# Performance work log

Hardware: AMD Instinct MI355X
Metric: run time of the kernel (lower is better)

Reference implementation:

```python
import jax, jax.numpy as jnp
import numpy as np

# Default widths from CWT.__init__: round((exp(linspace(0,2.5,5))-1)*30)+1
WIDTHS = [1, 27, 76, 167, 336]


def _morlet_int_psi():
    """pywt 'morl' wavelet: psi(t)=exp(-t^2/2)*cos(5t) on [-8,8], precision=10,
    integrated (cumulative) as in pywt.integrate_wavelet."""
    precision = 10
    n = 2 ** precision
    lb, ub = -8.0, 8.0
    t = np.linspace(lb, ub, n)
    psi = np.exp(-t ** 2 / 2.0) * np.cos(5.0 * t)
    step = t[1] - t[0]
    int_psi = np.cumsum(psi) * step
    return int_psi, step, lb, ub, n


def _filters(widths):
    """Per-scale resampled integrated wavelet, as in pywt.cwt.
    pywt uses np.convolve(data, int_psi[j][::-1]) (which flips its kernel);
    lax conv is a correlation (no flip), so the equivalent lax kernel is int_psi[j]."""
    int_psi, step, lb, ub, n = _morlet_int_psi()
    filts = []
    for scale in widths:
        j = (np.arange(scale * (ub - lb) + 1) / (scale * step)).astype(np.int64)
        j = j[j < n]
        filts.append(int_psi[j].astype(np.float32))
    return filts

_FILTERS = _filters(WIDTHS)


def _cwt_forward(x):
    # x: [N, T, C]; conv along T, channels independent
    N, T, C = x.shape
    xt = x.transpose(0, 2, 1).reshape(N * C, 1, T)  # [N*C, 1, T]
    outs = []
    for scale, f in zip(WIDTHS, _FILTERS):
        L = f.shape[0]
        k = jnp.asarray(f)[None, None, :]  # [out=1, in=1, L]
        # 'full' convolution: pad L-1 on each side
        conv = jax.lax.conv_general_dilated(xt, k, window_strides=(1,), padding=[(L - 1, L - 1)])  # [N*C,1,T+L-1]
        coef = (-np.sqrt(float(scale))) * jnp.diff(conv, axis=-1)  # [N*C,1,T+L-2]
        d = (coef.shape[-1] - T) / 2.0  # trim to central T samples (pywt)
        lo = int(np.floor(d))
        hi = coef.shape[-1] - int(np.ceil(d))
        coef = coef[..., lo:hi]  # [N*C, 1, T]
        outs.append(coef.reshape(N, C, T))
    out = jnp.stack(outs, axis=0)  # [F, N, C, T]
    return out.transpose(1, 3, 2, 0)  # [N, T, C, F]


def setup_inputs() -> dict:
    key = jax.random.key(0)
    x = jax.random.normal(key, (16, 2048, 64), dtype=jnp.float32)
    return {"x": x}


def reference(x):
    return _cwt_forward(x)
```

## Files before the change

kernel.cpp:

```cpp
#include <hip/hip_runtime.h>
#include <hip/hip_fp16.h>
#include <math.h>

#define NB    16
#define T     2048
#define NC    64
#define NROWS (NB*NC)
#define PADL2 2696
#define XSH_N 7440

#define WTOT_U4 19840

#define WS_XT    (1u<<19)
#define WS_OUTT  ((1u<<19) + (1u<<22))

typedef _Float16 half8  __attribute__((ext_vector_type(8)));
typedef _Float16 half4v __attribute__((ext_vector_type(4)));
typedef float    f32x4  __attribute__((ext_vector_type(4)));

__global__ __launch_bounds__(1024) void cwt_prep(const float* __restrict__ x,
                                                 __half* __restrict__ xT,
                                                 __half* __restrict__ W) {
    __shared__ double ps[1024];
    __shared__ double sc[1024];
    __shared__ float  k32[1024];
    __shared__ float  tile4[4][64 * 65];
    const int tid = threadIdx.x;

    if (blockIdx.x == 0) {
        uint4* W4 = (uint4*)W;
        const uint4 z = make_uint4(0u, 0u, 0u, 0u);
        for (int i = tid; i < WTOT_U4; i += 1024) W4[i] = z;

        const double delta = 16.0 / 1023.0;
        double t = (tid == 1023) ? 8.0 : (-8.0 + delta * (double)tid);
        ps[tid] = exp(-0.5 * t * t) * cos(5.0 * t);
        __syncthreads();

        double* a = ps; double* b = sc;
        for (int off = 1; off < 1024; off <<= 1) {
            double v = a[tid];
            if (tid >= off) v += a[tid - off];
            b[tid] = v;
            __syncthreads();
            double* tmp = a; a = b; b = tmp;
        }
        const double step = ((-8.0 + delta) + 8.0);
        k32[tid] = (float)(a[tid] * step);
        __syncthreads();

        constexpr int SCe[5]   = {336, 167, 76, 27, 1};
        constexpr int KS2[5]   = {5408, 2720, 1248, 480, 64};
        constexpr int WOFFe[5] = {0, 86528, 130048, 150016, 157696};
        constexpr int CLOe[5]  = {0, 42, 65, 77, 83};
        for (int sl = 0; sl < 5; ++sl) {
            const int s = SCe[sl];
            const int L = 16 * s + 1;
            const double c = (double)s * step;
            const float sq = (float)sqrt((double)s);
            const int posoff = PADL2 - 8 * s - 1;
            const int kb0 = posoff - 32 * CLOe[sl];
            __half* wb = W + WOFFe[sl];
            const int Ks = KS2[sl];
            for (int i = tid; i <= L; i += 1024) {
                float g; bool wr = true;
                if (i == 0) {
                    g = sq * k32[0];
                } else if (i == L) {
                    long long jl = (long long)((double)(L - 1) / c);
                    if (jl > 1023) jl = 1023;
                    g = -sq * k32[jl];
                } else {
                    long long j1 = (long long)((double)i / c);
                    long long j0 = (long long)((double)(i - 1) / c);
                    if (j1 > 1023) j1 = 1023;
                    if (j0 > 1023) j0 = 1023;
                    wr = (j1 > j0);
                    g = sq * (k32[j1] - k32[j0]);
                }
                if (wr) {
                    const __half hg = __float2half(g);
                    const int kb = kb0 + i;
                    #pragma unroll
                    for (int bb = 0; bb < 16; ++bb)
                        wb[bb * Ks + kb + bb] = hg;
                }
            }
        }
    } else {
        const int g    = tid >> 8;
        const int t256 = tid & 255;
        const int ti   = (blockIdx.x - 1) * 4 + g;
        const int n    = ti >> 5;
        const int t0   = (ti & 31) << 6;
        float* tl = tile4[g];

        const float4* src = (const float4*)(x + ((size_t)(n * T + t0)) * NC);
        #pragma unroll
        for (int k = 0; k < 4; ++k) {
            float4 v = src[t256 + 256 * k];
            const int flat = (t256 + 256 * k) * 4;
            const int tt = flat >> 6, c = flat & 63;
            tl[tt * 65 + c + 0] = v.x;
            tl[tt * 65 + c + 1] = v.y;
            tl[tt * 65 + c + 2] = v.z;
            tl[tt * 65 + c + 3] = v.w;
        }
        __syncthreads();
        const int lane = t256 & 63, w4 = t256 >> 6;
        for (int cc = w4; cc < 64; cc += 4) {
            xT[((size_t)(n * 64 + cc)) * T + t0 + lane] = __float2half(tl[lane * 65 + cc]);
        }
    }
}

template<int N, int DEPTH>
__device__ __forceinline__ void conv_seg(int c0, int c1,
                                         const _Float16* __restrict__ xb,
                                         const _Float16* const (&ap)[5],
                                         f32x4 (&acc)[5][4]) {
    half8 A[DEPTH][N];
    half8 B[DEPTH][4];
    #pragma unroll
    for (int d = 0; d < DEPTH; ++d) {
        const int ko = (c0 + d) << 5;
        #pragma unroll
        for (int sl = 0; sl < N; ++sl) A[d][sl] = *(const half8*)(ap[sl] + ko);
        #pragma unroll
        for (int j = 0; j < 4; ++j)   B[d][j]  = *(const half8*)(xb + 256 * j + ko);
    }
    int c = c0;
    for (; c + DEPTH <= c1; c += DEPTH) {
        #pragma unroll
        for (int d = 0; d < DEPTH; ++d) {
            #pragma unroll
            for (int sl = 0; sl < N; ++sl) {
                acc[sl][0] = __builtin_amdgcn_mfma_f32_16x16x32_f16(A[d][sl], B[d][0], acc[sl][0], 0, 0, 0);
                acc[sl][1] = __builtin_amdgcn_mfma_f32_16x16x32_f16(A[d][sl], B[d][1], acc[sl][1], 0, 0, 0);
                acc[sl][2] = __builtin_amdgcn_mfma_f32_16x16x32_f16(A[d][sl], B[d][2], acc[sl][2], 0, 0, 0);
                acc[sl][3] = __builtin_amdgcn_mfma_f32_16x16x32_f16(A[d][sl], B[d][3], acc[sl][3], 0, 0, 0);
            }
            const int ko = (c + DEPTH + d) << 5;
            #pragma unroll
            for (int sl = 0; sl < N; ++sl) A[d][sl] = *(const half8*)(ap[sl] + ko);
            #pragma unroll
            for (int j = 0; j < 4; ++j)   B[d][j]  = *(const half8*)(xb + 256 * j + ko);
        }
    }
    #pragma unroll
    for (int d = 0; d < DEPTH; ++d) {
        if (d < c1 - c) {
            #pragma unroll
            for (int sl = 0; sl < N; ++sl) {
                acc[sl][0] = __builtin_amdgcn_mfma_f32_16x16x32_f16(A[d][sl], B[d][0], acc[sl][0], 0, 0, 0);
                acc[sl][1] = __builtin_amdgcn_mfma_f32_16x16x32_f16(A[d][sl], B[d][1], acc[sl][1], 0, 0, 0);
                acc[sl][2] = __builtin_amdgcn_mfma_f32_16x16x32_f16(A[d][sl], B[d][2], acc[sl][2], 0, 0, 0);
                acc[sl][3] = __builtin_amdgcn_mfma_f32_16x16x32_f16(A[d][sl], B[d][3], acc[sl][3], 0, 0, 0);
            }
        }
    }
}

__global__ __launch_bounds__(128, 2) void cwt_conv_mfma(const __half* __restrict__ xT,
                                                        const __half* __restrict__ Wg,
                                                        __half* __restrict__ outT) {
    constexpr int KS2[5]   = {5408, 2720, 1248, 480, 64};
    constexpr int WOFFe[5] = {0, 86528, 130048, 150016, 157696};
    constexpr int CLOe[5]  = {0, 42, 65, 77, 83};
    constexpr int OS[5]    = {4, 3, 2, 1, 0};

    __shared__ _Float16 xsh[XSH_N];
    __shared__ _Float16 ostage[2048];
    const int tid  = threadIdx.x;
    const int row  = blockIdx.x;
    const int nidx = row >> 6;
    const int cidx = row & 63;
    const int lane = tid & 63;
    const int w    = tid >> 6;
    const int mcol = lane & 15;
    const int grp  = lane >> 4;

    {
        uint4* x4 = (uint4*)xsh;
        const uint4 z = make_uint4(0u, 0u, 0u, 0u);
        for (int i = tid; i < XSH_N / 8; i += 128)
            if (i < PADL2 / 8 || i >= (PADL2 + T) / 8) x4[i] = z;
        const uint4* src = (const uint4*)(xT + (size_t)row * T);
        x4[PADL2 / 8 + tid] = src[tid];
        x4[PADL2 / 8 + 128 + tid] = src[128 + tid];
    }
    __syncthreads();

    const _Float16* xb = xsh + 1024 * w + 16 * mcol + 8 * grp;
    const _Float16* ap[5];
    #pragma unroll
    for (int sl = 0; sl < 5; ++sl)
        ap[sl] = (const _Float16*)Wg + WOFFe[sl] + mcol * KS2[sl] + 8 * grp
                 - (CLOe[sl] << 5);

    f32x4 acc[5][4];
    #pragma unroll
    for (int sl = 0; sl < 5; ++sl)
        #pragma unroll
        for (int j = 0; j < 4; ++j)
            acc[sl][j] = (f32x4){0.f, 0.f, 0.f, 0.f};

    conv_seg<1,3>(  0,  42, xb, ap, acc);
    conv_seg<2,3>( 42,  65, xb, ap, acc);
    conv_seg<3,2>( 65,  77, xb, ap, acc);
    conv_seg<4,2>( 77,  83, xb, ap, acc);
    conv_seg<5,2>( 83,  85, xb, ap, acc);
    conv_seg<4,2>( 85,  92, xb, ap, acc);
    conv_seg<3,2>( 92, 104, xb, ap, acc);
    conv_seg<2,3>(104, 127, xb, ap, acc);
    conv_seg<1,3>(127, 169, xb, ap, acc);

    _Float16* os = ostage + 1024 * w;
    #pragma unroll
    for (int sl = 0; sl < 5; ++sl) {
        #pragma unroll
        for (int j = 0; j < 4; ++j) {
            half4v h;
            #pragma unroll
            for (int r = 0; r < 4; ++r) h[r] = (_Float16)acc[sl][j][r];
            *(half4v*)(os + 256 * j + 16 * mcol + 4 * grp) = h;
        }
        half8 o0 = *(const half8*)(os + 16 * lane);
        half8 o1 = *(const half8*)(os + 16 * lane + 8);
        __half* ob = outT + ((size_t)(((nidx * 128 + 64 * w + lane) * 64 + cidx) * 5 + OS[sl])) * 16;
        *(half8*)(ob)     = o0;
        *(half8*)(ob + 8) = o1;
    }
}

__global__ __launch_bounds__(256) void cwt_fix(const __half* __restrict__ outT,
                                               float* __restrict__ out) {
    __shared__ float tile[16 * 320];
    const int b  = blockIdx.x;
    const int n  = b >> 7;
    const int tb = b & 127;
    const int tid = threadIdx.x;

    const uint4* src = (const uint4*)(outT + (size_t)(n * 128 + tb) * 5120);
    for (int i = tid; i < 640; i += 256) {
        uint4 v = src[i];
        const __half* h = (const __half*)&v;
        const int h0  = i * 8;
        const int sg  = h0 >> 4;
        const int tt0 = h0 & 15;
        #pragma unroll
        for (int k = 0; k < 8; ++k) tile[(tt0 + k) * 320 + sg] = __half2float(h[k]);
    }
    __syncthreads();
    float4* dst = (float4*)(out + (size_t)(n * 2048 + tb * 16) * 320);
    const float4* tl = (const float4*)tile;
    for (int k = tid; k < 1280; k += 256) dst[k] = tl[k];
}

extern "C" void kernel_launch(void* const* d_in, const int* in_sizes, int n_in,
                              void* d_out, int out_size, void* d_ws, size_t ws_size,
                              hipStream_t stream) {
    const float* x = (const float*)d_in[0];
    float* out = (float*)d_out;
    char* ws = (char*)d_ws;

    __half* W    = (__half*)ws;
    __half* xT   = (__half*)(ws + WS_XT);
    __half* outT = (__half*)(ws + WS_OUTT);

    cwt_prep<<<129, 1024, 0, stream>>>(x, xT, W);
    cwt_conv_mfma<<<NROWS, 128, 0, stream>>>(xT, W, outT);
    cwt_fix<<<2048, 256, 0, stream>>>(outT, out);
}
```

Before: 143.5 us.

## Fuse output transpose into conv kernel, writing fp32 results directly

Removes the separate fix kernel and the fp16 intermediate buffer: the MFMA conv kernel now writes fp32 accumulators straight into the final [N,T,C,F] layout with scattered strided stores. It also raises the depth of the first and last conv segments from 3 to 5 and enlarges the shared x buffer, presumably so the deeper segments stay in bounds. This saves one launch and a round trip through global memory, but the direct stores are 4-byte writes at a 320-float stride across lanes, so they are poorly coalesced. Writing fp32 instead of fp16 also changes the output precision path.

```diff
diff --git a/kernel.cpp b/kernel.cpp
--- a/kernel.cpp
+++ b/kernel.cpp
@@ -7,15 +7,13 @@
 #define NC    64
 #define NROWS (NB*NC)
 #define PADL2 2696
-#define XSH_N 7440
+#define XSH_N 7600
 
 #define WTOT_U4 19840
 
 #define WS_XT    (1u<<19)
-#define WS_OUTT  ((1u<<19) + (1u<<22))
 
 typedef _Float16 half8  __attribute__((ext_vector_type(8)));
-typedef _Float16 half4v __attribute__((ext_vector_type(4)));
 typedef float    f32x4  __attribute__((ext_vector_type(4)));
 
 __global__ __launch_bounds__(1024) void cwt_prep(const float* __restrict__ x,
@@ -163,14 +161,12 @@
 
 __global__ __launch_bounds__(128, 2) void cwt_conv_mfma(const __half* __restrict__ xT,
                                                         const __half* __restrict__ Wg,
-                                                        __half* __restrict__ outT) {
+                                                        float* __restrict__ out) {
     constexpr int KS2[5]   = {5408, 2720, 1248, 480, 64};
     constexpr int WOFFe[5] = {0, 86528, 130048, 150016, 157696};
     constexpr int CLOe[5]  = {0, 42, 65, 77, 83};
-    constexpr int OS[5]    = {4, 3, 2, 1, 0};
 
     __shared__ _Float16 xsh[XSH_N];
-    __shared__ _Float16 ostage[2048];
     const int tid  = threadIdx.x;
     const int row  = blockIdx.x;
     const int nidx = row >> 6;
@@ -205,7 +201,7 @@
         for (int j = 0; j < 4; ++j)
             acc[sl][j] = (f32x4){0.f, 0.f, 0.f, 0.f};
 
-    conv_seg<1,3>(  0,  42, xb, ap, acc);
+    conv_seg<1,5>(  0,  42, xb, ap, acc);
     conv_seg<2,3>( 42,  65, xb, ap, acc);
     conv_seg<3,2>( 65,  77, xb, ap, acc);
     conv_seg<4,2>( 77,  83, xb, ap, acc);
@@ -213,48 +209,21 @@
     conv_seg<4,2>( 85,  92, xb, ap, acc);
     conv_seg<3,2>( 92, 104, xb, ap, acc);
     conv_seg<2,3>(104, 127, xb, ap, acc);
-    conv_seg<1,3>(127, 169, xb, ap, acc);
-
-    _Float16* os = ostage + 1024 * w;
-    #pragma unroll
-    for (int sl = 0; sl < 5; ++sl) {
-        #pragma unroll
-        for (int j = 0; j < 4; ++j) {
-            half4v h;
-            #pragma unroll
-            for (int r = 0; r < 4; ++r) h[r] = (_Float16)acc[sl][j][r];
-            *(half4v*)(os + 256 * j + 16 * mcol + 4 * grp) = h;
-        }
-        half8 o0 = *(const half8*)(os + 16 * lane);
-        half8 o1 = *(const half8*)(os + 16 * lane + 8);
-        __half* ob = outT + ((size_t)(((nidx * 128 + 64 * w + lane) * 64 + cidx) * 5 + OS[sl])) * 16;
-        *(half8*)(ob)     = o0;
-        *(half8*)(ob + 8) = o1;
-    }
-}
-
-__global__ __launch_bounds__(256) void cwt_fix(const __half* __restrict__ outT,
-                                               float* __restrict__ out) {
-    __shared__ float tile[16 * 320];
-    const int b  = blockIdx.x;
-    const int n  = b >> 7;
-    const int tb = b & 127;
-    const int tid = threadIdx.x;
-
-    const uint4* src = (const uint4*)(outT + (size_t)(n * 128 + tb) * 5120);
-    for (int i = tid; i < 640; i += 256) {
-        uint4 v = src[i];
-        const __half* h = (const __half*)&v;
-        const int h0  = i * 8;
-        const int sg  = h0 >> 4;
-        const int tt0 = h0 & 15;
-        #pragma unroll
-        for (int k = 0; k < 8; ++k) tile[(tt0 + k) * 320 + sg] = __half2float(h[k]);
-    }
-    __syncthreads();
-    float4* dst = (float4*)(out + (size_t)(n * 2048 + tb * 16) * 320);
-    const float4* tl = (const float4*)tile;
-    for (int k = tid; k < 1280; k += 256) dst[k] = tl[k];
+    conv_seg<1,5>(127, 169, xb, ap, acc);
+
+    #pragma unroll
+    for (int j = 0; j < 4; ++j) {
+        #pragma unroll
+        for (int r = 0; r < 4; ++r) {
+            const int t = 1024 * w + 256 * j + 16 * mcol + 4 * grp + r;
+            float* ob = out + ((size_t)((nidx * 2048 + t) * 64 + cidx)) * 5;
+            ob[4] = acc[0][j][r];
+            ob[3] = acc[1][j][r];
+            ob[2] = acc[2][j][r];
+            ob[1] = acc[3][j][r];
+            ob[0] = acc[4][j][r];
+        }
+    }
 }
 
 extern "C" void kernel_launch(void* const* d_in, const int* in_sizes, int n_in,
@@ -266,9 +235,7 @@
 
     __half* W    = (__half*)ws;
     __half* xT   = (__half*)(ws + WS_XT);
-    __half* outT = (__half*)(ws + WS_OUTT);
 
     cwt_prep<<<129, 1024, 0, stream>>>(x, xT, W);
-    cwt_conv_mfma<<<NROWS, 128, 0, stream>>>(xT, W, outT);
-    cwt_fix<<<2048, 256, 0, stream>>>(outT, out);
-}
+    cwt_conv_mfma<<<NROWS, 128, 0, stream>>>(xT, W, out);
+}
```

After: 170.3 us. 1.19x slower.
